# Optimization experiments

Measured on AMD Instinct MI355X. Metric: run time of the kernel, lower is better.

The kernel has to match this reference:

```python
import jax, jax.numpy as jnp
import numpy as np

N, E = 20000, 5000
IN_FT, OUT_FT = 128, 128
DENSITY = 0.01  # fraction of nonzeros in the incidence matrix


def setup_inputs() -> dict:
    key = jax.random.key(0)
    kx, kh, kw, kb = jax.random.split(key, 4)
    X = jax.random.normal(kx, (N, IN_FT), dtype=jnp.float32)
    H = (jax.random.uniform(kh, (N, E)) < DENSITY).astype(jnp.float32)
    # xavier_normal_ with gain=0.01
    xav_std = 0.01 * np.sqrt(2.0 / (IN_FT + OUT_FT))
    weight_trans = jax.random.normal(kw, (IN_FT, OUT_FT), dtype=jnp.float32) * xav_std
    bias = jax.random.normal(kb, (OUT_FT,), dtype=jnp.float32) * 0.01
    return {"X": X, "H": H, "weight_trans": weight_trans, "bias": bias}


def reference(X, H, weight_trans, bias):
    # X: [N, in_ft], H: [N, E] incidence
    Xw = X @ weight_trans                      # [N, out_ft]
    DV = jnp.sum(H, axis=1) + 1e-12            # node degrees, [N]
    DE = jnp.sum(H, axis=0) + 1e-12            # hyperedge degrees, [E]
    # G = diag(1/DV) @ H @ diag(1/DE) @ H^T applied to Xw, computed in the
    # efficient order without materializing the NxN matrix G:
    M = H.T @ Xw                               # [E, out_ft]
    M = M / DE[:, None]                        # diag(1/DE) scaling
    out = H @ M                                # [N, out_ft]
    out = out / DV[:, None]                    # diag(1/DV) scaling
    out = out + bias
    return jax.nn.relu(out)
```

## Files before the change

### kernel.cpp

```cpp
#include <hip/hip_runtime.h>
#include <hip/hip_bf16.h>

typedef unsigned long long u64;
typedef unsigned int u32;
typedef unsigned short u16;
typedef __attribute__((ext_vector_type(4))) float f32x4v;
typedef __attribute__((ext_vector_type(16))) float f32x16;
typedef __attribute__((ext_vector_type(8))) short bf16x8;

#define N_NODES 20000
#define N_EDGES 5000
#define FT 128
#define NT 20
#define NRG 313
#define ROW_U64 80
#define COL_STRIDE 5120
#define XWT_S 20032

#define NTLOAD(p) __builtin_nontemporal_load((const f32x4v*)(p))

static __device__ __forceinline__ u64 spread4(u64 x) {
  x = (x | (x << 24)) & 0x000000FF000000FFull;
  x = (x | (x << 12)) & 0x000F000F000F000Full;
  x = (x | (x << 6))  & 0x0303030303030303ull;
  x = (x | (x << 3))  & 0x1111111111111111ull;
  return x;
}

static __device__ __forceinline__ u16 f2bf(float x) {
  u32 u = __float_as_uint(x);
  u = (u + 0x7FFFu + ((u >> 16) & 1u)) >> 16;
  return (u16)u;
}

static __device__ __forceinline__ bf16x8 expand8(u32 b) {
  union { u32 u[4]; bf16x8 v; } r;
  r.u[0] = (( b        & 1u) | ((( b >> 1) & 1u) << 16)) * 0x3F80u;
  r.u[1] = (((b >> 2)  & 1u) | ((( b >> 3) & 1u) << 16)) * 0x3F80u;
  r.u[2] = (((b >> 4)  & 1u) | ((( b >> 5) & 1u) << 16)) * 0x3F80u;
  r.u[3] = (((b >> 6)  & 1u) | ((( b >> 7) & 1u) << 16)) * 0x3F80u;
  return r.v;
}

static __device__ __forceinline__ int swz(int c, int r) {
  return c * 256 + (((r + c) & 31) << 3);
}

__global__ __launch_bounds__(256) void scan_fused(
    const float* __restrict__ H, u64* __restrict__ Hbt, u64* __restrict__ HbtT,
    const float2* __restrict__ X2, __hip_bfloat162* __restrict__ Xb2,
    const float* __restrict__ Wf, u16* __restrict__ WtB) {
  const int wid = threadIdx.x >> 6, lane = threadIdx.x & 63;

  if (blockIdx.x >= 1565) {
    for (int i = (blockIdx.x - 1565) * 256 + threadIdx.x; i < 1280000;
         i += 320 * 256)
      Xb2[i] = __float22bfloat162_rn(X2[i]);
    if (blockIdx.x == 1884) {
      for (int i = threadIdx.x; i < FT * FT; i += 256) {
        int f = i >> 7, k = i & 127;
        WtB[i] = f2bf(Wf[k * FT + f]);
      }
    }
    return;
  }

  const int gw = blockIdx.x * 4 + wid;
  const int t = gw % NT, rg = gw / NT;
  const int r0 = rg * 64;
  const int rows = min(64, N_NODES - r0);
  const int idx4 = t * 64 + lane;
  const bool lv = idx4 < 1250;

  u64 m0 = 0, m1 = 0, m2 = 0, m3 = 0;
  for (int kb = 0; kb < rows; kb += 8) {
    f32x4v vv[8];
#pragma unroll
    for (int k = 0; k < 8; ++k) vv[k] = (f32x4v){0.f, 0.f, 0.f, 0.f};
    if (lv) {
      const float* bp = H + (size_t)(r0 + kb) * N_EDGES + idx4 * 4;
#pragma unroll
      for (int k = 0; k < 8; ++k) vv[k] = NTLOAD(bp + (size_t)k * N_EDGES);
    }
#pragma unroll
    for (int k = 0; k < 8; ++k) {
      u64 b0 = __ballot(vv[k].x != 0.f);
      u64 b1 = __ballot(vv[k].y != 0.f);
      u64 b2 = __ballot(vv[k].z != 0.f);
      u64 b3 = __ballot(vv[k].w != 0.f);
      const bool keep = (lane == kb + k);
      m0 = keep ? b0 : m0;  m1 = keep ? b1 : m1;
      m2 = keep ? b2 : m2;  m3 = keep ? b3 : m3;
    }
  }
  if (lane < rows) {
    u64* hp = Hbt + (size_t)(r0 + lane) * ROW_U64 + t * 4;
#pragma unroll
    for (int j = 0; j < 4; ++j) {
      u64 p = spread4((m0 >> (16 * j)) & 0xFFFFull)
            | (spread4((m1 >> (16 * j)) & 0xFFFFull) << 1)
            | (spread4((m2 >> (16 * j)) & 0xFFFFull) << 2)
            | (spread4((m3 >> (16 * j)) & 0xFFFFull) << 3);
      hp[j] = p;
    }
  }
  u64 t0 = 0, t1 = 0, t2 = 0, t3 = 0;
  for (int l = 0; l < 64; ++l) {
    u64 c0 = __ballot((m0 >> l) & 1ull);
    u64 c1 = __ballot((m1 >> l) & 1ull);
    u64 c2 = __ballot((m2 >> l) & 1ull);
    u64 c3 = __ballot((m3 >> l) & 1ull);
    const bool keep = (lane == l);
    t0 = keep ? c0 : t0;  t1 = keep ? c1 : t1;
    t2 = keep ? c2 : t2;  t3 = keep ? c3 : t3;
  }
  u64* op = HbtT + (size_t)rg * COL_STRIDE + t * 256 + 4 * lane;
  op[0] = t0; op[1] = t1; op[2] = t2; op[3] = t3;
}

__global__ __launch_bounds__(256) void gemm_xw(
    const u16* __restrict__ Xb, const u16* __restrict__ WtB,
    u16* __restrict__ XwT) {
  __shared__ u16 xt[4096];
  const int wave = threadIdx.x >> 6, lane = threadIdx.x & 63;
  const int col = lane & 31, half = lane >> 5;
  const int n0 = blockIdx.x * 32;
  const int f0 = wave * 32;
  if (n0 >= N_NODES) {
    if (lane < 32)
      for (int r = 0; r < 32; ++r)
        XwT[(size_t)(f0 + r) * XWT_S + n0 + lane] = 0;
    return;
  }
  {
    const int sn = threadIdx.x >> 3, sc = threadIdx.x & 7;
#pragma unroll
    for (int j = 0; j < 2; ++j) {
      bf16x8 v = *(const bf16x8*)(Xb + (size_t)(n0 + sn) * FT + (sc + 8 * j) * 8);
      *(bf16x8*)(xt + sn * 128 + (((sc + 8 * j) + sn) & 15) * 8) = v;
    }
  }
  __syncthreads();
  f32x16 acc;
#pragma unroll
  for (int i = 0; i < 16; ++i) acc[i] = 0.f;
#pragma unroll
  for (int kc = 0; kc < 16; kc += 2) {
    int c = kc + half;
    bf16x8 a = *(const bf16x8*)(WtB + (f0 + col) * FT + c * 8);
    bf16x8 b = *(const bf16x8*)(xt + col * 128 + ((c + col) & 15) * 8);
    acc = __builtin_amdgcn_mfma_f32_32x32x16_bf16(a, b, acc, 0, 0, 0);
  }
#pragma unroll
  for (int r = 0; r < 16; ++r) {
    int fr = (r & 3) + 8 * (r >> 2) + 4 * half;
    XwT[(size_t)(f0 + fr) * XWT_S + n0 + col] = f2bf(acc[r]);
  }
}

__global__ __launch_bounds__(256) void edge_gemm(
    const u16* __restrict__ XwT, const u64* __restrict__ HbtT,
    u16* __restrict__ MhT) {
  __shared__ u16 atile[4][2][2048];
  __shared__ float sdv[4][32];
  const int tid = threadIdx.x;
  const int wid = tid >> 6, lane = tid & 63;
  const int col = lane & 31, half = lane >> 5;

  const int et = blockIdx.x % 160, ft = blockIdx.x / 160;
  const int e0 = et * 32, f0 = ft * 32;
  const int ws_ = wid * 78 + (wid > 0 ? 1 : 0);
  const int we_ = ws_ + (wid == 0 ? 79 : 78);

  const int srow = lane >> 3, schunk = lane & 7;
  const u16* sgbase = XwT + (size_t)(f0 + srow) * XWT_S + schunk * 8;
  u16* buf0 = &atile[wid][0][0];
  u16* buf1 = &atile[wid][1][0];

  f32x16 acc;
#pragma unroll
  for (int i = 0; i < 16; ++i) acc[i] = 0.f;
  float dv = 0.f;

  {
    bf16x8 st[4];
#pragma unroll
    for (int j = 0; j < 4; ++j)
      st[j] = *(const bf16x8*)(sgbase + (size_t)(8 * j) * XWT_S + ws_ * 64);
#pragma unroll
    for (int j = 0; j < 4; ++j)
      *(bf16x8*)(buf0 + swz(schunk, srow + 8 * j)) = st[j];
  }
  u64 wA = HbtT[(size_t)ws_ * COL_STRIDE + e0 + col];

  int p = 0;
  for (int w = ws_; w < we_; ++w) {
    const int wn = (w + 1 < we_) ? w + 1 : w;
    bf16x8 nst[4];
#pragma unroll
    for (int j = 0; j < 4; ++j)
      nst[j] = *(const bf16x8*)(sgbase + (size_t)(8 * j) * XWT_S + wn * 64);
    u64 nA = HbtT[(size_t)wn * COL_STRIDE + e0 + col];

    const u16* ab = p ? buf1 : buf0;
#pragma unroll
    for (int q = 0; q < 4; ++q) {
      bf16x8 a = *(const bf16x8*)(ab + swz(2 * q + half, col));
      bf16x8 b = expand8((u32)(wA >> (q * 16 + half * 8)) & 0xFFu);
      acc = __builtin_amdgcn_mfma_f32_32x32x16_bf16(a, b, acc, 0, 0, 0);
    }
    dv += (float)__popcll(wA);

    u16* nb = p ? buf0 : buf1;
#pragma unroll
    for (int j = 0; j < 4; ++j)
      *(bf16x8*)(nb + swz(schunk, srow + 8 * j)) = nst[j];
    wA = nA; p ^= 1;
  }

  float* sacc = (float*)&atile[wid][0][0];
#pragma unroll
  for (int r = 0; r < 16; ++r) {
    int fr = (r & 3) + 8 * (r >> 2) + 4 * half;
    sacc[fr * 32 + col] = acc[r];
  }
  if (half == 0) sdv[wid][col] = dv;
  __syncthreads();

  {
    const int frl = tid >> 3, eq = tid & 7;
    const float* s0 = (const float*)&atile[0][0][0];
    union { u16 h[4]; u64 q; } o;
#pragma unroll
    for (int j = 0; j < 4; ++j) {
      int e = eq * 4 + j;
      int idx = frl * 32 + e;
      float s = s0[idx] + s0[2048 + idx] + s0[4096 + idx] + s0[6144 + idx];
      float d = sdv[0][e] + sdv[1][e] + sdv[2][e] + sdv[3][e];
      o.h[j] = f2bf(s / (d + 1e-12f));
    }
    *(u64*)(MhT + (size_t)(f0 + frl) * COL_STRIDE + e0 + eq * 4) = o.q;
  }
}

__global__ __launch_bounds__(256) void node_gemm(
    const u64* __restrict__ Hbt, const u16* __restrict__ MhT,
    const float* __restrict__ bias, float* __restrict__ out) {
  __shared__ u16 btile[4][2][2048];
  const int tid = threadIdx.x;
  const int wid = tid >> 6, lane = tid & 63;
  const int col = lane & 31, half = lane >> 5;
  const int n0 = blockIdx.x * 32;
  const int f0 = wid * 32;

  const int srow = lane >> 3, schunk = lane & 7;
  const u16* sgbase = MhT + (size_t)(f0 + srow) * COL_STRIDE + schunk * 8;
  u16* buf0 = &btile[wid][0][0];
  u16* buf1 = &btile[wid][1][0];

  f32x16 acc;
#pragma unroll
  for (int i = 0; i < 16; ++i) acc[i] = 0.f;

  {
    bf16x8 st[4];
#pragma unroll
    for (int j = 0; j < 4; ++j)
      st[j] = *(const bf16x8*)(sgbase + (size_t)(8 * j) * COL_STRIDE);
#pragma unroll
    for (int j = 0; j < 4; ++j)
      *(bf16x8*)(buf0 + swz(schunk, srow + 8 * j)) = st[j];
  }
  u64 word = Hbt[(size_t)(n0 + col) * ROW_U64];
  float dv = 0.f;

  int p = 0;
  for (int w = 0; w < ROW_U64; ++w) {
    const int wn = (w + 1 < ROW_U64) ? w + 1 : w;
    bf16x8 nst[4];
#pragma unroll
    for (int j = 0; j < 4; ++j)
      nst[j] = *(const bf16x8*)(sgbase + (size_t)(8 * j) * COL_STRIDE + wn * 64);
    u64 nword = Hbt[(size_t)(n0 + col) * ROW_U64 + wn];

    const u16* bb = p ? buf1 : buf0;
#pragma unroll
    for (int q = 0; q < 4; ++q) {
      bf16x8 a = expand8((u32)(word >> (q * 16 + half * 8)) & 0xFFu);
      bf16x8 b = *(const bf16x8*)(bb + swz(2 * q + half, col));
      acc = __builtin_amdgcn_mfma_f32_32x32x16_bf16(a, b, acc, 0, 0, 0);
    }
    dv += (float)__popcll(word);

    u16* nb = p ? buf0 : buf1;
#pragma unroll
    for (int j = 0; j < 4; ++j)
      *(bf16x8*)(nb + swz(schunk, srow + 8 * j)) = nst[j];
    word = nword; p ^= 1;
  }

  float inv = 1.f / (dv + 1e-12f);
  float bb = bias[f0 + col];
#pragma unroll
  for (int r = 0; r < 16; ++r) {
    int rr = (r & 3) + 8 * (r >> 2) + 4 * half;
    float iv = __shfl(inv, rr);
    out[(size_t)(n0 + rr) * FT + f0 + col] = fmaxf(fmaf(acc[r], iv, bb), 0.f);
  }
}

extern "C" void kernel_launch(void* const* d_in, const int* in_sizes, int n_in,
                              void* d_out, int out_size, void* d_ws, size_t ws_size,
                              hipStream_t stream) {
  const float* X    = (const float*)d_in[0];
  const float* H    = (const float*)d_in[1];
  const float* W    = (const float*)d_in[2];
  const float* bias = (const float*)d_in[3];
  float* out = (float*)d_out;

  int* ws = (int*)d_ws;
  u64* Hbt             = (u64*)ws;
  u64* HbtT            = (u64*)(ws + 3200000);
  __hip_bfloat162* Xb2 = (__hip_bfloat162*)(ws + 6405120);
  u16* MhT             = (u16*)(ws + 6405120);
  u16* WtB             = (u16*)(ws + 7685120);
  u16* XwT             = (u16*)(ws + 7693312);

  scan_fused<<<1885, 256, 0, stream>>>(H, Hbt, HbtT, (const float2*)X, Xb2,
                                       W, WtB);
  gemm_xw   <<<626, 256, 0, stream>>>((const u16*)Xb2, WtB, XwT);
  edge_gemm <<<640, 256, 0, stream>>>(XwT, HbtT, MhT);
  node_gemm <<<625, 256, 0, stream>>>(Hbt, MhT, bias, out);
}
```

Measured before the change: 646.9 us.

## Prefetch two stages ahead in edge/node GEMMs and transpose node bitmask layout

The edge and node GEMM main loops now issue global loads two iterations ahead, using a register triple-buffer that feeds the LDS double buffer, so there is more time to hide memory latency. The node bitmask array is stored word-major ([word][node]) rather than node-major. This makes each word load in node_gemm coalesced across the 32 columns. In exchange, scan_fused's stores of that array become strided, and extra registers are used for the deeper prefetch.

```diff
diff --git a/kernel.cpp b/kernel.cpp
--- a/kernel.cpp
+++ b/kernel.cpp
@@ -47,7 +47,7 @@
 }
 
 __global__ __launch_bounds__(256) void scan_fused(
-    const float* __restrict__ H, u64* __restrict__ Hbt, u64* __restrict__ HbtT,
+    const float* __restrict__ H, u64* __restrict__ Hbt2, u64* __restrict__ HbtT,
     const float2* __restrict__ X2, __hip_bfloat162* __restrict__ Xb2,
     const float* __restrict__ Wf, u16* __restrict__ WtB) {
   const int wid = threadIdx.x >> 6, lane = threadIdx.x & 63;
@@ -94,14 +94,13 @@
     }
   }
   if (lane < rows) {
-    u64* hp = Hbt + (size_t)(r0 + lane) * ROW_U64 + t * 4;
 #pragma unroll
     for (int j = 0; j < 4; ++j) {
       u64 p = spread4((m0 >> (16 * j)) & 0xFFFFull)
             | (spread4((m1 >> (16 * j)) & 0xFFFFull) << 1)
             | (spread4((m2 >> (16 * j)) & 0xFFFFull) << 2)
             | (spread4((m3 >> (16 * j)) & 0xFFFFull) << 3);
-      hp[j] = p;
+      Hbt2[(size_t)(t * 4 + j) * N_NODES + (r0 + lane)] = p;
     }
   }
   u64 t0 = 0, t1 = 0, t2 = 0, t3 = 0;
@@ -182,40 +181,47 @@
   for (int i = 0; i < 16; ++i) acc[i] = 0.f;
   float dv = 0.f;
 
+  bf16x8 rB[4], rC[4];
   {
-    bf16x8 st[4];
-#pragma unroll
-    for (int j = 0; j < 4; ++j)
-      st[j] = *(const bf16x8*)(sgbase + (size_t)(8 * j) * XWT_S + ws_ * 64);
-#pragma unroll
-    for (int j = 0; j < 4; ++j)
-      *(bf16x8*)(buf0 + swz(schunk, srow + 8 * j)) = st[j];
-  }
-  u64 wA = HbtT[(size_t)ws_ * COL_STRIDE + e0 + col];
+    const int w1 = (ws_ + 1 < we_) ? ws_ + 1 : ws_;
+    bf16x8 rA[4];
+#pragma unroll
+    for (int j = 0; j < 4; ++j)
+      rA[j] = *(const bf16x8*)(sgbase + (size_t)(8 * j) * XWT_S + ws_ * 64);
+#pragma unroll
+    for (int j = 0; j < 4; ++j)
+      rB[j] = *(const bf16x8*)(sgbase + (size_t)(8 * j) * XWT_S + w1 * 64);
+#pragma unroll
+    for (int j = 0; j < 4; ++j)
+      *(bf16x8*)(buf0 + swz(schunk, srow + 8 * j)) = rA[j];
+  }
+  u64 h0 = HbtT[(size_t)ws_ * COL_STRIDE + e0 + col];
+  u64 h1 = HbtT[(size_t)((ws_ + 1 < we_) ? ws_ + 1 : ws_) * COL_STRIDE + e0 + col];
 
   int p = 0;
   for (int w = ws_; w < we_; ++w) {
-    const int wn = (w + 1 < we_) ? w + 1 : w;
-    bf16x8 nst[4];
-#pragma unroll
-    for (int j = 0; j < 4; ++j)
-      nst[j] = *(const bf16x8*)(sgbase + (size_t)(8 * j) * XWT_S + wn * 64);
-    u64 nA = HbtT[(size_t)wn * COL_STRIDE + e0 + col];
+    const int w2 = (w + 2 < we_) ? w + 2 : we_ - 1;
+#pragma unroll
+    for (int j = 0; j < 4; ++j)
+      rC[j] = *(const bf16x8*)(sgbase + (size_t)(8 * j) * XWT_S + w2 * 64);
+    u64 h2 = HbtT[(size_t)w2 * COL_STRIDE + e0 + col];
 
     const u16* ab = p ? buf1 : buf0;
 #pragma unroll
     for (int q = 0; q < 4; ++q) {
       bf16x8 a = *(const bf16x8*)(ab + swz(2 * q + half, col));
-      bf16x8 b = expand8((u32)(wA >> (q * 16 + half * 8)) & 0xFFu);
+      bf16x8 b = expand8((u32)(h0 >> (q * 16 + half * 8)) & 0xFFu);
       acc = __builtin_amdgcn_mfma_f32_32x32x16_bf16(a, b, acc, 0, 0, 0);
     }
-    dv += (float)__popcll(wA);
+    dv += (float)__popcll(h0);
 
     u16* nb = p ? buf0 : buf1;
 #pragma unroll
     for (int j = 0; j < 4; ++j)
-      *(bf16x8*)(nb + swz(schunk, srow + 8 * j)) = nst[j];
-    wA = nA; p ^= 1;
+      *(bf16x8*)(nb + swz(schunk, srow + 8 * j)) = rB[j];
+#pragma unroll
+    for (int j = 0; j < 4; ++j) rB[j] = rC[j];
+    h0 = h1; h1 = h2; p ^= 1;
   }
 
   float* sacc = (float*)&atile[wid][0][0];
@@ -244,7 +250,7 @@
 }
 
 __global__ __launch_bounds__(256) void node_gemm(
-    const u64* __restrict__ Hbt, const u16* __restrict__ MhT,
+    const u64* __restrict__ Hbt2, const u16* __restrict__ MhT,
     const float* __restrict__ bias, float* __restrict__ out) {
   __shared__ u16 btile[4][2][2048];
   const int tid = threadIdx.x;
@@ -261,42 +267,48 @@
   f32x16 acc;
 #pragma unroll
   for (int i = 0; i < 16; ++i) acc[i] = 0.f;
-
+  float dv = 0.f;
+
+  bf16x8 rB[4], rC[4];
   {
-    bf16x8 st[4];
-#pragma unroll
-    for (int j = 0; j < 4; ++j)
-      st[j] = *(const bf16x8*)(sgbase + (size_t)(8 * j) * COL_STRIDE);
-#pragma unroll
-    for (int j = 0; j < 4; ++j)
-      *(bf16x8*)(buf0 + swz(schunk, srow + 8 * j)) = st[j];
-  }
-  u64 word = Hbt[(size_t)(n0 + col) * ROW_U64];
-  float dv = 0.f;
+    bf16x8 rA[4];
+#pragma unroll
+    for (int j = 0; j < 4; ++j)
+      rA[j] = *(const bf16x8*)(sgbase + (size_t)(8 * j) * COL_STRIDE);
+#pragma unroll
+    for (int j = 0; j < 4; ++j)
+      rB[j] = *(const bf16x8*)(sgbase + (size_t)(8 * j) * COL_STRIDE + 64);
+#pragma unroll
+    for (int j = 0; j < 4; ++j)
+      *(bf16x8*)(buf0 + swz(schunk, srow + 8 * j)) = rA[j];
+  }
+  u64 h0 = Hbt2[(size_t)0 * N_NODES + n0 + col];
+  u64 h1 = Hbt2[(size_t)1 * N_NODES + n0 + col];
 
   int p = 0;
   for (int w = 0; w < ROW_U64; ++w) {
-    const int wn = (w + 1 < ROW_U64) ? w + 1 : w;
-    bf16x8 nst[4];
-#pragma unroll
-    for (int j = 0; j < 4; ++j)
-      nst[j] = *(const bf16x8*)(sgbase + (size_t)(8 * j) * COL_STRIDE + wn * 64);
-    u64 nword = Hbt[(size_t)(n0 + col) * ROW_U64 + wn];
+    const int w2 = (w + 2 < ROW_U64) ? w + 2 : ROW_U64 - 1;
+#pragma unroll
+    for (int j = 0; j < 4; ++j)
+      rC[j] = *(const bf16x8*)(sgbase + (size_t)(8 * j) * COL_STRIDE + w2 * 64);
+    u64 h2 = Hbt2[(size_t)w2 * N_NODES + n0 + col];
 
     const u16* bb = p ? buf1 : buf0;
 #pragma unroll
     for (int q = 0; q < 4; ++q) {
-      bf16x8 a = expand8((u32)(word >> (q * 16 + half * 8)) & 0xFFu);
+      bf16x8 a = expand8((u32)(h0 >> (q * 16 + half * 8)) & 0xFFu);
       bf16x8 b = *(const bf16x8*)(bb + swz(2 * q + half, col));
       acc = __builtin_amdgcn_mfma_f32_32x32x16_bf16(a, b, acc, 0, 0, 0);
     }
-    dv += (float)__popcll(word);
+    dv += (float)__popcll(h0);
 
     u16* nb = p ? buf0 : buf1;
 #pragma unroll
     for (int j = 0; j < 4; ++j)
-      *(bf16x8*)(nb + swz(schunk, srow + 8 * j)) = nst[j];
-    word = nword; p ^= 1;
+      *(bf16x8*)(nb + swz(schunk, srow + 8 * j)) = rB[j];
+#pragma unroll
+    for (int j = 0; j < 4; ++j) rB[j] = rC[j];
+    h0 = h1; h1 = h2; p ^= 1;
   }
 
   float inv = 1.f / (dv + 1e-12f);
@@ -319,16 +331,16 @@
   float* out = (float*)d_out;
 
   int* ws = (int*)d_ws;
-  u64* Hbt             = (u64*)ws;
+  u64* Hbt2            = (u64*)ws;
   u64* HbtT            = (u64*)(ws + 3200000);
   __hip_bfloat162* Xb2 = (__hip_bfloat162*)(ws + 6405120);
   u16* MhT             = (u16*)(ws + 6405120);
   u16* WtB             = (u16*)(ws + 7685120);
   u16* XwT             = (u16*)(ws + 7693312);
 
-  scan_fused<<<1885, 256, 0, stream>>>(H, Hbt, HbtT, (const float2*)X, Xb2,
+  scan_fused<<<1885, 256, 0, stream>>>(H, Hbt2, HbtT, (const float2*)X, Xb2,
                                        W, WtB);
   gemm_xw   <<<626, 256, 0, stream>>>((const u16*)Xb2, WtB, XwT);
   edge_gemm <<<640, 256, 0, stream>>>(XwT, HbtT, MhT);
-  node_gemm <<<625, 256, 0, stream>>>(Hbt, MhT, bias, out);
-}
+  node_gemm <<<625, 256, 0, stream>>>(Hbt2, MhT, bias, out);
+}
```

Result: no change. 653.5 us (+1.0%).
